# Kernel tuning notes

Hardware: AMD Instinct MI355X
Metric: run time of the kernel (lower is better)

The kernel has to match this reference:

```python
import jax, jax.numpy as jnp
import numpy as np

B, L, ENC, H, E, V, T = 128, 196, 512, 512, 256, 10000, 20


def setup_inputs() -> dict:
    key = jax.random.key(0)
    ks = jax.random.split(key, 24)
    s = 0.02
    n = lambda k, shp: jax.random.normal(k, shp, jnp.float32) * s
    return {
        'img_feat': jax.random.normal(ks[0], (B, L, ENC), jnp.float32),
        'W_h': n(ks[1], (ENC, H)), 'b_h': jnp.zeros((H,), jnp.float32),
        'W_c': n(ks[2], (ENC, H)), 'b_c': jnp.zeros((H,), jnp.float32),
        'W_gate': n(ks[3], (H, ENC)), 'b_gate': jnp.zeros((ENC,), jnp.float32),
        'emb': n(ks[4], (V, E)),
        'W_ae': n(ks[5], (ENC, H)), 'b_ae': jnp.zeros((H,), jnp.float32),
        'W_ad': n(ks[6], (H, H)), 'b_ad': jnp.zeros((H,), jnp.float32),
        'v_att': n(ks[7], (H,)), 'b_v': jnp.zeros((), jnp.float32),
        'W_ih': n(ks[8], (E + ENC, 4 * H)), 'b_ih': jnp.zeros((4 * H,), jnp.float32),
        'W_hh': n(ks[9], (H, 4 * H)), 'b_hh': jnp.zeros((4 * H,), jnp.float32),
        'W_out': n(ks[10], (H, V)), 'b_out': jnp.zeros((V,), jnp.float32),
        'captions': jax.random.randint(ks[11], (B, T), 0, V),
        'max_len': T,
    }


def reference(img_feat, W_h, b_h, W_c, b_c, W_gate, b_gate, emb,
              W_ae, b_ae, W_ad, b_ad, v_att, b_v,
              W_ih, b_ih, W_hh, b_hh, W_out, b_out,
              captions, max_len):
    feat_mean = img_feat.mean(axis=1)                       # [B, ENC]
    h0 = jnp.tanh(feat_mean @ W_h + b_h)                    # [B, H]
    c0 = jnp.tanh(feat_mean @ W_c + b_c)                    # [B, H]
    enc_proj = jnp.einsum('ble,ea->bla', img_feat, W_ae) + b_ae  # [B, L, H]
    emb_seq = emb[captions]                                 # [B, T, E]
    xs = jnp.swapaxes(emb_seq, 0, 1)[:max_len]              # [T, B, E]

    def step(carry, x_t):
        h, c = carry
        # Bahdanau attention
        dec_proj = (h @ W_ad + b_ad)[:, None, :]            # [B, 1, H]
        e = jnp.tanh(enc_proj + dec_proj) @ v_att + b_v     # [B, L]
        alpha = jax.nn.softmax(e, axis=-1)                  # [B, L]
        context = jnp.einsum('bl,ble->be', alpha, img_feat) # [B, ENC]
        gate = jax.nn.sigmoid(h @ W_gate + b_gate)          # [B, ENC]
        x = jnp.concatenate([x_t, context * gate], axis=1)  # [B, E+ENC]
        gates = x @ W_ih + h @ W_hh + (b_ih + b_hh)         # [B, 4H]
        i, f, g, o = jnp.split(gates, 4, axis=1)
        c_new = jax.nn.sigmoid(f) * c + jax.nn.sigmoid(i) * jnp.tanh(g)
        h_new = jax.nn.sigmoid(o) * jnp.tanh(c_new)
        # dropout is identity in eval mode
        out = h_new @ W_out + b_out                         # [B, V]
        return (h_new, c_new), (out, alpha)

    _, (outs, alphas) = jax.lax.scan(step, (h0, c0), xs)
    return jnp.swapaxes(outs, 0, 1), jnp.swapaxes(alphas, 0, 1)
```

## Files before the change

### kernel.cpp

```cpp
#include <hip/hip_runtime.h>
#include <math.h>

typedef unsigned short ushort_t;
typedef __attribute__((ext_vector_type(8))) short bf16x8;
typedef __attribute__((ext_vector_type(4))) short bf16x4;
typedef __attribute__((ext_vector_type(4))) float f32x4;

constexpr int Bb  = 128;
constexpr int Ll  = 196;
constexpr int ENCe= 512;
constexpr int Hh  = 512;
constexpr int Ee  = 256;
constexpr int Vv  = 10000;
constexpr int Tt  = 20;

#define DEV __device__ __forceinline__

DEV float sigm_f(float x) { return 1.f / (1.f + __expf(-x)); }
DEV float tanh_f(float x) {
    x = fminf(fmaxf(x, -15.f), 15.f);
    float e = __expf(2.f * x);
    return (e - 1.f) / (e + 1.f);
}
DEV ushort_t f2bf(float v) {
    unsigned u = __float_as_uint(v);
    return (ushort_t)((u + 0x7FFFu + ((u >> 16) & 1u)) >> 16);
}
DEV float bf2f(ushort_t h) { return __uint_as_float(((unsigned)h) << 16); }

DEV void store_xh(ushort_t* __restrict__ H, ushort_t* __restrict__ L,
                  int b, int k, float v)
{
    size_t idx = (((size_t)(b >> 4) * 40 + (k >> 5)) * 64
                  + ((k >> 3) & 3) * 16 + (b & 15)) * 8 + (k & 7);
    ushort_t hb = f2bf(v);
    H[idx] = hb;
    L[idx] = f2bf(v - bf2f(hb));
}

template<int BN, int TM, int TN, int ACT1, int OUTBF>
__global__ __launch_bounds__(256)
void gemm_k(const float* __restrict__ A, int lda,
            const float* __restrict__ Wk, int ldw,
            const float* __restrict__ bias,
            void* __restrict__ Cv, long long ldc,
            int M, int N, int K)
{
    constexpr int BM = 64, BK = 16;
    constexpr int TX = BN / TN, TY = BM / TM;
    static_assert(TX * TY == 256, "bad tile config");
    __shared__ float As[BK][BM];
    __shared__ float Ws[BK][BN];

    const int tid = threadIdx.x;
    const int tx = tid % TX, ty = tid / TX;
    const int nb = blockIdx.x * BN, mb = blockIdx.y * BM;

    float acc[TM][TN] = {};
    const int am = tid >> 2;
    const int ak = (tid & 3) * 4;
    const int wn = tid % BN;
    const int wk0 = tid / BN;
    constexpr int WKSTEP = 256 / BN;

    for (int k0 = 0; k0 < K; k0 += BK) {
        float4 av = *(const float4*)&A[(size_t)(mb + am) * lda + k0 + ak];
        As[ak + 0][am] = av.x;
        As[ak + 1][am] = av.y;
        As[ak + 2][am] = av.z;
        As[ak + 3][am] = av.w;
        #pragma unroll
        for (int i = 0; i < BK / WKSTEP; ++i) {
            int kw = wk0 + i * WKSTEP;
            Ws[kw][wn] = (nb + wn < N) ? Wk[(size_t)(k0 + kw) * ldw + nb + wn] : 0.f;
        }
        __syncthreads();
        #pragma unroll
        for (int k = 0; k < BK; ++k) {
            float a[TM], w[TN];
            #pragma unroll
            for (int i = 0; i < TM; ++i) a[i] = As[k][ty * TM + i];
            #pragma unroll
            for (int j = 0; j < TN; ++j) w[j] = Ws[k][tx * TN + j];
            #pragma unroll
            for (int i = 0; i < TM; ++i)
                #pragma unroll
                for (int j = 0; j < TN; ++j)
                    acc[i][j] = fmaf(a[i], w[j], acc[i][j]);
        }
        __syncthreads();
    }

    #pragma unroll
    for (int i = 0; i < TM; ++i) {
        int m = mb + ty * TM + i;
        #pragma unroll
        for (int j = 0; j < TN; ++j) {
            int n = nb + tx * TN + j;
            if (n < N) {
                float v = acc[i][j];
                if (bias) v += bias[n];
                if (ACT1 == 1) v = tanh_f(v);
                if (OUTBF) ((ushort_t*)Cv)[(size_t)m * ldc + n] = f2bf(v);
                else       ((float*)Cv)[(size_t)m * ldc + n] = v;
            }
        }
    }
}

template<int MT, int NT, int ACT1, int ACT2, int SPLIT, bool OUTBF, bool PERM,
         bool XSWZ, bool NMINOR, bool W2D>
__global__ __launch_bounds__(256)
void mgemm_pk(const ushort_t* __restrict__ AH, const ushort_t* __restrict__ AL, int aFS,
              const ushort_t* __restrict__ BH, const ushort_t* __restrict__ BL, int bFS,
              const float* __restrict__ bias, const float* __restrict__ bias2, int N1,
              void* __restrict__ Cv, long long ldc, long long ldc2,
              int Nfrags, int Ntot, int nsteps, int bdiv)
{
    int bx, by;
    if (XSWZ) {
        int nwg = gridDim.x, orig = blockIdx.x;
        int xcd = orig & 7, idx = orig >> 3;
        int q = nwg >> 3, r = nwg & 7;
        int lin = (xcd < r ? xcd * (q + 1) : r * (q + 1) + (xcd - r) * q) + idx;
        int l1 = lin / bdiv, l2 = lin - l1 * bdiv;
        bx = NMINOR ? l2 : l1;
        by = NMINOR ? l1 : l2;
    } else { bx = blockIdx.x; by = blockIdx.y; }

    const int wv = threadIdx.x >> 6, lane = threadIdx.x & 63;
    int nf0, mf0;
    if (W2D) {
        nf0 = (bx * 2 + (wv & 1)) * NT;
        mf0 = by * (2 * MT) + (wv >> 1) * MT;
    } else {
        nf0 = (bx * 4 + wv) * NT;
        mf0 = by * MT;
    }
    if (nf0 >= Nfrags) return;
    const int col = lane & 15;
    const int lofs = lane * 8;

    const ushort_t *paH[MT], *paL[MT], *pbH[NT], *pbL[NT];
    #pragma unroll
    for (int mt = 0; mt < MT; ++mt) {
        paH[mt] = AH + (size_t)(mf0 + mt) * aFS + lofs;
        paL[mt] = (SPLIT >= 2) ? (AL + (size_t)(mf0 + mt) * aFS + lofs) : paH[mt];
    }
    #pragma unroll
    for (int ct = 0; ct < NT; ++ct) {
        int nf = nf0 + ct; if (nf > Nfrags - 1) nf = Nfrags - 1;
        pbH[ct] = BH + (size_t)nf * bFS + lofs;
        pbL[ct] = (SPLIT == 3) ? (BL + (size_t)nf * bFS + lofs) : pbH[ct];
    }

    f32x4 acc[MT][NT];
    #pragma unroll
    for (int mt = 0; mt < MT; ++mt)
        #pragma unroll
        for (int ct = 0; ct < NT; ++ct) acc[mt][ct] = (f32x4){0.f, 0.f, 0.f, 0.f};

    auto LOADF = [&](bf16x8 (&A0)[MT], bf16x8 (&A1)[MT],
                     bf16x8 (&B0)[NT], bf16x8 (&B1)[NT], int i) {
        size_t o = (size_t)i * 512;
        #pragma unroll
        for (int mt = 0; mt < MT; ++mt) {
            A0[mt] = *(const bf16x8*)(paH[mt] + o);
            if (SPLIT >= 2) A1[mt] = *(const bf16x8*)(paL[mt] + o);
        }
        #pragma unroll
        for (int ct = 0; ct < NT; ++ct) {
            B0[ct] = *(const bf16x8*)(pbH[ct] + o);
            if (SPLIT == 3) B1[ct] = *(const bf16x8*)(pbL[ct] + o);
        }
    };
    auto COMPF = [&](bf16x8 (&A0)[MT], bf16x8 (&A1)[MT],
                     bf16x8 (&B0)[NT], bf16x8 (&B1)[NT]) {
        #pragma unroll
        for (int mt = 0; mt < MT; ++mt)
            #pragma unroll
            for (int ct = 0; ct < NT; ++ct) {
                acc[mt][ct] = __builtin_amdgcn_mfma_f32_16x16x32_bf16(A0[mt], B0[ct], acc[mt][ct], 0, 0, 0);
                if (SPLIT >= 2)
                    acc[mt][ct] = __builtin_amdgcn_mfma_f32_16x16x32_bf16(A1[mt], B0[ct], acc[mt][ct], 0, 0, 0);
                if (SPLIT == 3)
                    acc[mt][ct] = __builtin_amdgcn_mfma_f32_16x16x32_bf16(A0[mt], B1[ct], acc[mt][ct], 0, 0, 0);
            }
    };

    bf16x8 xa0[MT], xa1[MT], xb0[NT], xb1[NT];
    bf16x8 ya0[MT], ya1[MT], yb0[NT], yb1[NT];
    LOADF(xa0, xa1, xb0, xb1, 0);
    for (int i = 0; i < nsteps; i += 2) {
        LOADF(ya0, ya1, yb0, yb1, i + 1);
        COMPF(xa0, xa1, xb0, xb1);
        if (i + 2 < nsteps) LOADF(xa0, xa1, xb0, xb1, i + 2);
        COMPF(ya0, ya1, yb0, yb1);
    }

    #pragma unroll
    for (int ct = 0; ct < NT; ++ct) {
        const int nc = (nf0 + ct) * 16 + col;
        if (nc >= Ntot) continue;
        const bool ns = ((nf0 + ct) * 16 >= N1);
        float bv = ns ? (bias2 ? bias2[nc - N1] : 0.f) : (bias ? bias[nc] : 0.f);
        const int act = ns ? ACT2 : ACT1;
        #pragma unroll
        for (int mt = 0; mt < MT; ++mt)
            #pragma unroll
            for (int r = 0; r < 4; ++r) {
                int row = (mf0 + mt) * 16 + (lane >> 4) * 4 + r;
                float v = acc[mt][ct][r] + bv;
                if (act == 1)      v = tanh_f(v);
                else if (act == 2) v = sigm_f(v);
                size_t off = PERM ? ((size_t)(row & 127) * ldc + (size_t)(row >> 7) * ldc2 + nc)
                                  : ((size_t)row * ldc + nc);
                if (OUTBF)      ((ushort_t*)Cv)[off] = f2bf(v);
                else if (PERM)  __builtin_nontemporal_store(v, &((float*)Cv)[off]);
                else            ((float*)Cv)[off] = v;
            }
    }
}

template<bool LO>
__global__ __launch_bounds__(256)
void convT_pk(const float* __restrict__ W, int N, int KSr,
              ushort_t* __restrict__ PH, ushort_t* __restrict__ PL,
              int KSfull, int ksOfs, int nfOfs)
{
    int tid = blockIdx.x * 256 + threadIdx.x;
    int lane = tid & 63;
    int rest = tid >> 6;
    int ks = rest % KSr;
    int nf = rest / KSr;
    const float* src = W + (size_t)(ks * 32 + ((lane >> 4) & 3) * 8) * N
                         + nf * 16 + (lane & 15);
    size_t dbase = (((size_t)(nf + nfOfs) * KSfull + ks + ksOfs) * 64 + lane) * 8;
    #pragma unroll
    for (int jj = 0; jj < 8; ++jj) {
        float v = src[(size_t)jj * N];
        ushort_t h = f2bf(v);
        PH[dbase + jj] = h;
        if (LO) PL[dbase + jj] = f2bf(v - bf2f(h));
    }
}

__global__ __launch_bounds__(256)
void convimg_k(const float* __restrict__ img, ushort_t* __restrict__ linH,
               ushort_t* __restrict__ pkH)
{
    int tid = blockIdx.x * 256 + threadIdx.x;
    int lane = tid & 63;
    int rest = tid >> 6;
    int ks = rest & 15, rf = rest >> 4;
    int r = rf * 16 + (lane & 15);
    int k = ks * 32 + ((lane >> 4) & 3) * 8;
    const float* src = img + (size_t)r * 512 + k;
    ushort_t* ld = linH + (size_t)r * 512 + k;
    size_t pidx = (((size_t)rf * 16 + ks) * 64 + lane) * 8;
    #pragma unroll
    for (int jj = 0; jj < 8; ++jj) {
        ushort_t h = f2bf(src[jj]);
        ld[jj] = h;
        pkH[pidx + jj] = h;
    }
}

__global__ void convbf_k(const float* __restrict__ src, ushort_t* __restrict__ dst,
                         long long n)
{
    long long i = (long long)(blockIdx.x * 256 + threadIdx.x) * 4;
    long long stride = (long long)gridDim.x * 1024;
    for (; i + 3 < n; i += stride) {
        float4 v = *(const float4*)&src[i];
        dst[i + 0] = f2bf(v.x); dst[i + 1] = f2bf(v.y);
        dst[i + 2] = f2bf(v.z); dst[i + 3] = f2bf(v.w);
    }
}

__global__ __launch_bounds__(256)
void featmean_k(const float* __restrict__ img, float* __restrict__ fm)
{
    int b = blockIdx.x, tid = threadIdx.x;
    const float* base = img + (size_t)b * Ll * ENCe;
    for (int e = tid; e < ENCe; e += 256) {
        float s = 0.f;
        for (int l = 0; l < Ll; ++l) s += base[l * ENCe + e];
        fm[b * ENCe + e] = s * (1.f / (float)Ll);
    }
}

__global__ void bcomb_k(const float* __restrict__ bih, const float* __restrict__ bhh,
                        float* __restrict__ bc)
{
    int i = blockIdx.x * 256 + threadIdx.x;
    if (i < 4 * Hh) bc[i] = bih[i] + bhh[i];
}

__global__ void hconv_k(const float* __restrict__ h, ushort_t* __restrict__ xhi,
                        ushort_t* __restrict__ xlo)
{
    int i = blockIdx.x * 256 + threadIdx.x;
    if (i >= Bb * Hh) return;
    int b = i / Hh, j = i % Hh;
    store_xh(xhi, xlo, b, 768 + j, h[i]);
}

struct LP {
    const ushort_t *WdgH, *WdgL, *WgH, *WgL;
    const float    *b_ad, *b_gate, *bcomb;
    float          *dgb, *cbuf;
    ushort_t       *xhH, *xhL, *hsH, *hsL;
};

__global__ __launch_bounds__(256)
void ph_dg_k(LP P)
{
    __shared__ f32x4 part[2][64];
    const int beta = blockIdx.x;
    const int tid = threadIdx.x, wv = tid >> 6, lane = tid & 63;
    const int bx = beta >> 3, mf = beta & 7;
    const int nf = bx * 2 + (wv & 1), kh = wv >> 1;
    const int lofs = lane * 8;
    const bool blo = (P.WdgL != nullptr);

    const ushort_t* paH = P.xhH + ((size_t)mf * 40 + 24 + kh * 8) * 512 + lofs;
    const ushort_t* paL = P.xhL + ((size_t)mf * 40 + 24 + kh * 8) * 512 + lofs;
    const ushort_t* pbH = P.WdgH + ((size_t)nf * 16 + kh * 8) * 512 + lofs;
    const ushort_t* pbL = blo ? (P.WdgL + ((size_t)nf * 16 + kh * 8) * 512 + lofs) : pbH;

    f32x4 acc = (f32x4){0.f, 0.f, 0.f, 0.f};
    #pragma unroll
    for (int i = 0; i < 8; ++i) {
        size_t o = (size_t)i * 512;
        bf16x8 A0 = *(const bf16x8*)(paH + o);
        bf16x8 A1 = *(const bf16x8*)(paL + o);
        bf16x8 B0 = *(const bf16x8*)(pbH + o);
        acc = __builtin_amdgcn_mfma_f32_16x16x32_bf16(A0, B0, acc, 0, 0, 0);
        acc = __builtin_amdgcn_mfma_f32_16x16x32_bf16(A1, B0, acc, 0, 0, 0);
        if (blo) {
            bf16x8 B1 = *(const bf16x8*)(pbL + o);
            acc = __builtin_amdgcn_mfma_f32_16x16x32_bf16(A0, B1, acc, 0, 0, 0);
        }
    }

    if (kh == 1) part[wv & 1][lane] = acc;
    __syncthreads();
    if (kh == 0) {
        acc += part[wv & 1][lane];
        int n = nf * 16 + (lane & 15);
        float bv = (n < 512) ? P.b_ad[n] : P.b_gate[n - 512];
        #pragma unroll
        for (int r = 0; r < 4; ++r) {
            int row = mf * 16 + (lane >> 4) * 4 + r;
            float v = acc[r] + bv;
            if (n >= 512) v = sigm_f(v);
            P.dgb[row * 1024 + n] = v;
        }
    }
}

template<bool IMGBF>
__global__ __launch_bounds__(512)
void attn_fused_k(const ushort_t* __restrict__ enc, const float* __restrict__ dgb,
                  const float* __restrict__ v_att,
                  const ushort_t* __restrict__ img_bf, const float* __restrict__ img_f,
                  const float* __restrict__ emb, const int* __restrict__ captions,
                  float* __restrict__ alphas, long long alpha_stride,
                  ushort_t* __restrict__ xhi, ushort_t* __restrict__ xlo, int t)
{
    int b = blockIdx.x, tid = threadIdx.x;
    int wv = tid >> 6, ln = tid & 63;
    __shared__ float es[Ll], red[8];
    __shared__ float ctxp[4][ENCe];

    float dp_r[8], va_r[8];
    {
        const float4* dptr = (const float4*)(dgb + b * 1024 + ln * 8);
        const float4* vptr = (const float4*)(v_att + ln * 8);
        float4 d0 = dptr[0], d1 = dptr[1];
        float4 v0 = vptr[0], v1 = vptr[1];
        dp_r[0] = d0.x; dp_r[1] = d0.y; dp_r[2] = d0.z; dp_r[3] = d0.w;
        dp_r[4] = d1.x; dp_r[5] = d1.y; dp_r[6] = d1.z; dp_r[7] = d1.w;
        va_r[0] = v0.x; va_r[1] = v0.y; va_r[2] = v0.z; va_r[3] = v0.w;
        va_r[4] = v1.x; va_r[5] = v1.y; va_r[6] = v1.z; va_r[7] = v1.w;
    }

    const ushort_t* ep = enc + (size_t)b * Ll * Hh;
    for (int l = wv; l < Ll; l += 8) {
        bf16x8 v8 = *(const bf16x8*)(ep + (size_t)l * Hh + ln * 8);
        float s = 0.f;
        #pragma unroll
        for (int j = 0; j < 8; ++j)
            s += tanh_f(bf2f((ushort_t)v8[j]) + dp_r[j]) * va_r[j];
        #pragma unroll
        for (int o = 32; o; o >>= 1) s += __shfl_xor(s, o);
        if (ln == 0) es[l] = s;
    }
    __syncthreads();

    float v = (tid < Ll) ? es[tid] : -1e30f;
    float m = v;
    #pragma unroll
    for (int o = 32; o; o >>= 1) m = fmaxf(m, __shfl_xor(m, o));
    if (ln == 0) red[wv] = m;
    __syncthreads();
    m = red[0];
    #pragma unroll
    for (int i = 1; i < 8; ++i) m = fmaxf(m, red[i]);
    __syncthreads();
    float p = (tid < Ll) ? __expf(v - m) : 0.f;
    float s = p;
    #pragma unroll
    for (int o = 32; o; o >>= 1) s += __shfl_xor(s, o);
    if (ln == 0) red[wv] = s;
    __syncthreads();
    s = 0.f;
    #pragma unroll
    for (int i = 0; i < 8; ++i) s += red[i];
    float inv = 1.f / s;
    if (tid < Ll) {
        float a = p * inv;
        es[tid] = a;
        alphas[(size_t)b * alpha_stride + tid] = a;
    }
    if (tid < Ee) {
        float xv = emb[(size_t)captions[b * Tt + t] * Ee + tid];
        store_xh(xhi, xlo, b, tid, xv);
    }
    __syncthreads();

    {
        const int g = tid >> 7, tl = tid & 127;
        const int l0 = g * 49;
        float a0 = 0.f, a1 = 0.f, a2 = 0.f, a3 = 0.f;
        if (IMGBF) {
            const ushort_t* ib = img_bf + (size_t)b * Ll * ENCe + tl * 4;
            for (int i = 0; i < 49; ++i) {
                float al = es[l0 + i];
                bf16x4 u = *(const bf16x4*)(ib + (size_t)(l0 + i) * ENCe);
                a0 = fmaf(al, bf2f((ushort_t)u[0]), a0);
                a1 = fmaf(al, bf2f((ushort_t)u[1]), a1);
                a2 = fmaf(al, bf2f((ushort_t)u[2]), a2);
                a3 = fmaf(al, bf2f((ushort_t)u[3]), a3);
            }
        } else {
            const float* ib = img_f + (size_t)b * Ll * ENCe + tl * 4;
            for (int i = 0; i < 49; ++i) {
                float al = es[l0 + i];
                float4 u = *(const float4*)(ib + (size_t)(l0 + i) * ENCe);
                a0 = fmaf(al, u.x, a0);
                a1 = fmaf(al, u.y, a1);
                a2 = fmaf(al, u.z, a2);
                a3 = fmaf(al, u.w, a3);
            }
        }
        f32x4 pv = (f32x4){a0, a1, a2, a3};
        *(f32x4*)&ctxp[g][tl * 4] = pv;
    }
    __syncthreads();

    {
        float cv = ctxp[0][tid] + ctxp[1][tid] + ctxp[2][tid] + ctxp[3][tid];
        float xv = cv * dgb[b * 1024 + 512 + tid];
        store_xh(xhi, xlo, b, 256 + tid, xv);
    }
}

__global__ __launch_bounds__(256)
void ph_gates_k(LP P, int t)
{
    __shared__ f32x4 part[3][4][64];
    const int beta = blockIdx.x;
    const int tid = threadIdx.x, wv = tid >> 6, lane = tid & 63;
    const int jf = beta & 31, mq = beta >> 5;
    const int ks0 = wv * 10, lofs = lane * 8;
    const bool blo = (P.WgL != nullptr);
    constexpr int FS = 40 * 512;

    const ushort_t* paH = P.xhH + ((size_t)mq * 40 + ks0) * 512 + lofs;
    const ushort_t* paL = P.xhL + ((size_t)mq * 40 + ks0) * 512 + lofs;
    const ushort_t *pbH[4], *pbL[4];
    #pragma unroll
    for (int g = 0; g < 4; ++g) {
        size_t off = (size_t)(g * 32 + jf) * FS + (size_t)ks0 * 512 + lofs;
        pbH[g] = P.WgH + off;
        pbL[g] = blo ? (P.WgL + off) : (P.WgH + off);
    }

    f32x4 acc[4];
    #pragma unroll
    for (int g = 0; g < 4; ++g) acc[g] = (f32x4){0.f, 0.f, 0.f, 0.f};

    auto LOADF = [&](bf16x8 (&A)[2], bf16x8 (&B)[4][2], int i) {
        size_t o = (size_t)i * 512;
        A[0] = *(const bf16x8*)(paH + o);
        A[1] = *(const bf16x8*)(paL + o);
        #pragma unroll
        for (int g = 0; g < 4; ++g) {
            B[g][0] = *(const bf16x8*)(pbH[g] + o);
            if (blo) B[g][1] = *(const bf16x8*)(pbL[g] + o);
        }
    };
    auto COMPF = [&](bf16x8 (&A)[2], bf16x8 (&B)[4][2]) {
        #pragma unroll
        for (int g = 0; g < 4; ++g) {
            acc[g] = __builtin_amdgcn_mfma_f32_16x16x32_bf16(A[0], B[g][0], acc[g], 0, 0, 0);
            acc[g] = __builtin_amdgcn_mfma_f32_16x16x32_bf16(A[1], B[g][0], acc[g], 0, 0, 0);
            if (blo)
                acc[g] = __builtin_amdgcn_mfma_f32_16x16x32_bf16(A[0], B[g][1], acc[g], 0, 0, 0);
        }
    };

    bf16x8 xA[2], xB[4][2], yA[2], yB[4][2];
    LOADF(xA, xB, 0);
    for (int i = 0; i < 10; i += 2) {
        LOADF(yA, yB, i + 1);
        COMPF(xA, xB);
        if (i + 2 < 10) LOADF(xA, xB, i + 2);
        COMPF(yA, yB);
    }

    if (wv > 0) {
        #pragma unroll
        for (int g = 0; g < 4; ++g) part[wv - 1][g][lane] = acc[g];
    }
    __syncthreads();
    if (wv == 0) {
        #pragma unroll
        for (int g = 0; g < 4; ++g) {
            acc[g] += part[0][g][lane];
            acc[g] += part[1][g][lane];
            acc[g] += part[2][g][lane];
        }
        const int j = jf * 16 + (lane & 15);
        float bi = P.bcomb[j], bf_ = P.bcomb[512 + j];
        float bg = P.bcomb[1024 + j], bo = P.bcomb[1536 + j];
        #pragma unroll
        for (int r = 0; r < 4; ++r) {
            int b = mq * 16 + (lane >> 4) * 4 + r;
            float ig = sigm_f(acc[0][r] + bi);
            float fg = sigm_f(acc[1][r] + bf_);
            float gg = tanh_f(acc[2][r] + bg);
            float og = sigm_f(acc[3][r] + bo);
            float cn = fg * P.cbuf[b * 512 + j] + ig * gg;
            P.cbuf[b * 512 + j] = cn;
            float hv = og * tanh_f(cn);
            store_xh(P.xhH, P.xhL, b, 768 + j, hv);
            ushort_t hb = f2bf(hv);
            size_t hidx = (((size_t)(t * 8 + (b >> 4)) * 16 + (j >> 5)) * 64
                           + ((j >> 3) & 3) * 16 + (b & 15)) * 8 + (j & 7);
            P.hsH[hidx] = hb;
            P.hsL[hidx] = f2bf(hv - bf2f(hb));
        }
    }
}

extern "C" void kernel_launch(void* const* d_in, const int* in_sizes, int n_in,
                              void* d_out, int out_size, void* d_ws, size_t ws_size,
                              hipStream_t stream)
{
    const float* img    = (const float*)d_in[0];
    const float* W_h    = (const float*)d_in[1];
    const float* b_h    = (const float*)d_in[2];
    const float* W_c    = (const float*)d_in[3];
    const float* b_c    = (const float*)d_in[4];
    const float* W_gate = (const float*)d_in[5];
    const float* b_gate = (const float*)d_in[6];
    const float* emb    = (const float*)d_in[7];
    const float* W_ae   = (const float*)d_in[8];
    const float* b_ae   = (const float*)d_in[9];
    const float* W_ad   = (const float*)d_in[10];
    const float* b_ad   = (const float*)d_in[11];
    const float* v_att  = (const float*)d_in[12];
    const float* W_ih   = (const float*)d_in[14];
    const float* b_ih   = (const float*)d_in[15];
    const float* W_hh   = (const float*)d_in[16];
    const float* b_hh   = (const float*)d_in[17];
    const float* W_out  = (const float*)d_in[18];
    const float* b_out  = (const float*)d_in[19];
    const int* captions = (const int*)d_in[20];

    float* out    = (float*)d_out;
    float* alphas = out + (size_t)Bb * Tt * Vv;

    char* p = (char*)d_ws;
    auto alloc = [&](size_t bytes) -> char* {
        char* r = p; p += (bytes + 255) & ~(size_t)255; return r;
    };
    const size_t szEnc   = (size_t)Bb * Ll * Hh * 2;
    const size_t szWout  = (size_t)625 * 16 * 512 * 2;
    const size_t szWg    = (size_t)128 * 40 * 512 * 2;
    const size_t szWdg   = (size_t)64 * 16 * 512 * 2;
    const size_t szWae   = (size_t)32 * 16 * 512 * 2;
    const size_t szXh    = (size_t)8 * 40 * 512 * 2;
    const size_t szHseq  = (size_t)160 * 16 * 512 * 2;
    const size_t szImg   = (size_t)Bb * Ll * ENCe * 2;

    ushort_t* enc_hi  = (ushort_t*)alloc(szEnc);
    ushort_t* WoutPkH = (ushort_t*)alloc(szWout);
    ushort_t* WgPkH   = (ushort_t*)alloc(szWg);
    ushort_t* WdgPkH  = (ushort_t*)alloc(szWdg);
    ushort_t* WaePkH  = (ushort_t*)alloc(szWae);
    ushort_t* xhPkH   = (ushort_t*)alloc(szXh);
    ushort_t* xhPkL   = (ushort_t*)alloc(szXh);
    ushort_t* hseqPkH = (ushort_t*)alloc(szHseq);
    ushort_t* hseqPkL = (ushort_t*)alloc(szHseq);
    float*    cbuf    = (float*)alloc((size_t)Bb * Hh * 4);
    float*    dgb     = (float*)alloc((size_t)Bb * 1024 * 4);
    float*    S       = (float*)alloc((size_t)Bb * 1024 * 4);
    float*    bcomb   = (float*)alloc(4 * Hh * 4);

    auto tryAlloc = [&](size_t bytes) -> char* {
        size_t used = (size_t)(p - (char*)d_ws);
        size_t rounded = (bytes + 255) & ~(size_t)255;
        if (used + rounded > ws_size) return nullptr;
        return alloc(bytes);
    };
    ushort_t* WoutPkL = (ushort_t*)tryAlloc(szWout);
    ushort_t* WgPkL   = (ushort_t*)tryAlloc(szWg);
    ushort_t* WdgPkL  = (ushort_t*)tryAlloc(szWdg);
    ushort_t* imgLin  = (ushort_t*)tryAlloc(szImg);
    ushort_t* imgPk   = (ushort_t*)tryAlloc(szImg);

    float* fm  = S;
    float* h0b = S + Bb * ENCe;

    dim3 blk(256);
    const int NOSPLIT = 0x40000000;
    const int aFSh    = 16 * 512;

    if (WoutPkL) convT_pk<true ><<<2500, blk, 0, stream>>>(W_out, Vv, 16, WoutPkH, WoutPkL, 16, 0, 0);
    else         convT_pk<false><<<2500, blk, 0, stream>>>(W_out, Vv, 16, WoutPkH, nullptr, 16, 0, 0);
    if (WgPkL) {
        convT_pk<true ><<<768, blk, 0, stream>>>(W_ih, 2048, 24, WgPkH, WgPkL, 40, 0, 0);
        convT_pk<true ><<<512, blk, 0, stream>>>(W_hh, 2048, 16, WgPkH, WgPkL, 40, 24, 0);
    } else {
        convT_pk<false><<<768, blk, 0, stream>>>(W_ih, 2048, 24, WgPkH, nullptr, 40, 0, 0);
        convT_pk<false><<<512, blk, 0, stream>>>(W_hh, 2048, 16, WgPkH, nullptr, 40, 24, 0);
    }
    if (WdgPkL) {
        convT_pk<true ><<<128, blk, 0, stream>>>(W_ad,   Hh, 16, WdgPkH, WdgPkL, 16, 0, 0);
        convT_pk<true ><<<128, blk, 0, stream>>>(W_gate, Hh, 16, WdgPkH, WdgPkL, 16, 0, 32);
    } else {
        convT_pk<false><<<128, blk, 0, stream>>>(W_ad,   Hh, 16, WdgPkH, nullptr, 16, 0, 0);
        convT_pk<false><<<128, blk, 0, stream>>>(W_gate, Hh, 16, WdgPkH, nullptr, 16, 0, 32);
    }
    convT_pk<false><<<128, blk, 0, stream>>>(W_ae, Hh, 16, WaePkH, nullptr, 16, 0, 0);

    bcomb_k<<<(4 * Hh + 255) / 256, blk, 0, stream>>>(b_ih, b_hh, bcomb);
    featmean_k<<<Bb, blk, 0, stream>>>(img, fm);

    gemm_k<32, 2, 4, 1, 0><<<dim3(Hh / 32, Bb / 64), blk, 0, stream>>>(
        fm, ENCe, W_h, Hh, b_h, h0b, Hh, Bb, Hh, ENCe);
    gemm_k<32, 2, 4, 1, 0><<<dim3(Hh / 32, Bb / 64), blk, 0, stream>>>(
        fm, ENCe, W_c, Hh, b_c, cbuf, Hh, Bb, Hh, ENCe);
    hconv_k<<<(Bb * Hh + 255) / 256, blk, 0, stream>>>(h0b, xhPkH, xhPkL);

    if (imgPk && imgLin) {
        convimg_k<<<6272, blk, 0, stream>>>(img, imgLin, imgPk);
        mgemm_pk<4, 4, 0, 0, 1, true, false, true, true, true><<<dim3(784), blk, 0, stream>>>(
            imgPk, nullptr, aFSh, WaePkH, nullptr, aFSh, b_ae, nullptr, NOSPLIT,
            enc_hi, Hh, 0, 32, Hh, 16, 4);
    } else {
        if (imgLin) convbf_k<<<2048, blk, 0, stream>>>(img, imgLin, (long long)Bb * Ll * ENCe);
        gemm_k<64, 4, 4, 0, 1><<<dim3(Hh / 64, (Bb * Ll) / 64), blk, 0, stream>>>(
            img, ENCe, W_ae, Hh, b_ae, enc_hi, Hh, Bb * Ll, Hh, ENCe);
    }

    LP P;
    P.WdgH = WdgPkH; P.WdgL = WdgPkL; P.WgH = WgPkH; P.WgL = WgPkL;
    P.b_ad = b_ad; P.b_gate = b_gate; P.bcomb = bcomb;
    P.dgb = dgb; P.cbuf = cbuf;
    P.xhH = xhPkH; P.xhL = xhPkL; P.hsH = hseqPkH; P.hsL = hseqPkL;

    for (int t = 0; t < Tt; ++t) {
        ph_dg_k<<<256, blk, 0, stream>>>(P);
        if (imgLin)
            attn_fused_k<true ><<<Bb, dim3(512), 0, stream>>>(
                enc_hi, dgb, v_att, imgLin, nullptr, emb, captions,
                alphas + (size_t)t * Ll, (long long)Tt * Ll, xhPkH, xhPkL, t);
        else
            attn_fused_k<false><<<Bb, dim3(512), 0, stream>>>(
                enc_hi, dgb, v_att, nullptr, img, emb, captions,
                alphas + (size_t)t * Ll, (long long)Tt * Ll, xhPkH, xhPkL, t);
        ph_gates_k<<<256, blk, 0, stream>>>(P, t);
    }

    if (WoutPkL)
        mgemm_pk<4, 4, 0, 0, 3, false, true, true, false, true><<<dim3(79 * 20), blk, 0, stream>>>(
            hseqPkH, hseqPkL, aFSh, WoutPkH, WoutPkL, aFSh,
            b_out, nullptr, NOSPLIT, out, (long long)Tt * Vv, (long long)Vv,
            625, Vv, 16, 20);
    else
        mgemm_pk<4, 4, 0, 0, 2, false, true, true, false, true><<<dim3(79 * 20), blk, 0, stream>>>(
            hseqPkH, hseqPkL, aFSh, WoutPkH, nullptr, aFSh,
            b_out, nullptr, NOSPLIT, out, (long long)Tt * Vv, (long long)Vv,
            625, Vv, 16, 20);
}
```

Measured before the change: 1.107 ms.

## Drop bf16 low-part weight splits and fuse small prologue kernels

```diff
diff --git a/kernel.cpp b/kernel.cpp
--- a/kernel.cpp
+++ b/kernel.cpp
@@ -104,6 +104,69 @@
                 if (OUTBF) ((ushort_t*)Cv)[(size_t)m * ldc + n] = f2bf(v);
                 else       ((float*)Cv)[(size_t)m * ldc + n] = v;
             }
+        }
+    }
+}
+
+__global__ __launch_bounds__(256)
+void gemmxh_k(const float* __restrict__ A, int lda,
+              const float* __restrict__ Wk, int ldw,
+              const float* __restrict__ bias,
+              ushort_t* __restrict__ xhH, ushort_t* __restrict__ xhL,
+              int N, int K)
+{
+    constexpr int BM = 64, BK = 16, BN = 32, TM = 2, TN = 4;
+    constexpr int TX = BN / TN;
+    __shared__ float As[BK][BM];
+    __shared__ float Ws[BK][BN];
+
+    const int tid = threadIdx.x;
+    const int tx = tid % TX, ty = tid / TX;
+    const int nb = blockIdx.x * BN, mb = blockIdx.y * BM;
+
+    float acc[TM][TN] = {};
+    const int am = tid >> 2;
+    const int ak = (tid & 3) * 4;
+    const int wn = tid % BN;
+    const int wk0 = tid / BN;
+    constexpr int WKSTEP = 256 / BN;
+
+    for (int k0 = 0; k0 < K; k0 += BK) {
+        float4 av = *(const float4*)&A[(size_t)(mb + am) * lda + k0 + ak];
+        As[ak + 0][am] = av.x;
+        As[ak + 1][am] = av.y;
+        As[ak + 2][am] = av.z;
+        As[ak + 3][am] = av.w;
+        #pragma unroll
+        for (int i = 0; i < BK / WKSTEP; ++i) {
+            int kw = wk0 + i * WKSTEP;
+            Ws[kw][wn] = Wk[(size_t)(k0 + kw) * ldw + nb + wn];
+        }
+        __syncthreads();
+        #pragma unroll
+        for (int k = 0; k < BK; ++k) {
+            float a[TM], w[TN];
+            #pragma unroll
+            for (int i = 0; i < TM; ++i) a[i] = As[k][ty * TM + i];
+            #pragma unroll
+            for (int j = 0; j < TN; ++j) w[j] = Ws[k][tx * TN + j];
+            #pragma unroll
+            for (int i = 0; i < TM; ++i)
+                #pragma unroll
+                for (int j = 0; j < TN; ++j)
+                    acc[i][j] = fmaf(a[i], w[j], acc[i][j]);
+        }
+        __syncthreads();
+    }
+
+    #pragma unroll
+    for (int i = 0; i < TM; ++i) {
+        int m = mb + ty * TM + i;
+        #pragma unroll
+        for (int j = 0; j < TN; ++j) {
+            int n = nb + tx * TN + j;
+            float v = tanh_f(acc[i][j] + bias[n]);
+            store_xh(xhH, xhL, m, 768 + n, v);
         }
     }
 }
@@ -279,9 +342,15 @@
 }
 
 __global__ __launch_bounds__(256)
-void featmean_k(const float* __restrict__ img, float* __restrict__ fm)
+void featmean_k(const float* __restrict__ img, float* __restrict__ fm,
+                const float* __restrict__ bih, const float* __restrict__ bhh,
+                float* __restrict__ bc)
 {
     int b = blockIdx.x, tid = threadIdx.x;
+    if (b < 8) {
+        int i = b * 256 + tid;
+        bc[i] = bih[i] + bhh[i];
+    }
     const float* base = img + (size_t)b * Ll * ENCe;
     for (int e = tid; e < ENCe; e += 256) {
         float s = 0.f;
@@ -290,24 +359,8 @@
     }
 }
 
-__global__ void bcomb_k(const float* __restrict__ bih, const float* __restrict__ bhh,
-                        float* __restrict__ bc)
-{
-    int i = blockIdx.x * 256 + threadIdx.x;
-    if (i < 4 * Hh) bc[i] = bih[i] + bhh[i];
-}
-
-__global__ void hconv_k(const float* __restrict__ h, ushort_t* __restrict__ xhi,
-                        ushort_t* __restrict__ xlo)
-{
-    int i = blockIdx.x * 256 + threadIdx.x;
-    if (i >= Bb * Hh) return;
-    int b = i / Hh, j = i % Hh;
-    store_xh(xhi, xlo, b, 768 + j, h[i]);
-}
-
 struct LP {
-    const ushort_t *WdgH, *WdgL, *WgH, *WgL;
+    const ushort_t *WdgH, *WgH;
     const float    *b_ad, *b_gate, *bcomb;
     float          *dgb, *cbuf;
     ushort_t       *xhH, *xhL, *hsH, *hsL;
@@ -322,12 +375,10 @@
     const int bx = beta >> 3, mf = beta & 7;
     const int nf = bx * 2 + (wv & 1), kh = wv >> 1;
     const int lofs = lane * 8;
-    const bool blo = (P.WdgL != nullptr);
 
     const ushort_t* paH = P.xhH + ((size_t)mf * 40 + 24 + kh * 8) * 512 + lofs;
     const ushort_t* paL = P.xhL + ((size_t)mf * 40 + 24 + kh * 8) * 512 + lofs;
     const ushort_t* pbH = P.WdgH + ((size_t)nf * 16 + kh * 8) * 512 + lofs;
-    const ushort_t* pbL = blo ? (P.WdgL + ((size_t)nf * 16 + kh * 8) * 512 + lofs) : pbH;
 
     f32x4 acc = (f32x4){0.f, 0.f, 0.f, 0.f};
     #pragma unroll
@@ -338,10 +389,6 @@
         bf16x8 B0 = *(const bf16x8*)(pbH + o);
         acc = __builtin_amdgcn_mfma_f32_16x16x32_bf16(A0, B0, acc, 0, 0, 0);
         acc = __builtin_amdgcn_mfma_f32_16x16x32_bf16(A1, B0, acc, 0, 0, 0);
-        if (blo) {
-            bf16x8 B1 = *(const bf16x8*)(pbL + o);
-            acc = __builtin_amdgcn_mfma_f32_16x16x32_bf16(A0, B1, acc, 0, 0, 0);
-        }
     }
 
     if (kh == 1) part[wv & 1][lane] = acc;
@@ -470,49 +517,40 @@
 __global__ __launch_bounds__(256)
 void ph_gates_k(LP P, int t)
 {
-    __shared__ f32x4 part[3][4][64];
+    __shared__ f32x4 part[4][4][64];
     const int beta = blockIdx.x;
     const int tid = threadIdx.x, wv = tid >> 6, lane = tid & 63;
     const int jf = beta & 31, mq = beta >> 5;
     const int ks0 = wv * 10, lofs = lane * 8;
-    const bool blo = (P.WgL != nullptr);
     constexpr int FS = 40 * 512;
 
     const ushort_t* paH = P.xhH + ((size_t)mq * 40 + ks0) * 512 + lofs;
     const ushort_t* paL = P.xhL + ((size_t)mq * 40 + ks0) * 512 + lofs;
-    const ushort_t *pbH[4], *pbL[4];
-    #pragma unroll
-    for (int g = 0; g < 4; ++g) {
-        size_t off = (size_t)(g * 32 + jf) * FS + (size_t)ks0 * 512 + lofs;
-        pbH[g] = P.WgH + off;
-        pbL[g] = blo ? (P.WgL + off) : (P.WgH + off);
-    }
+    const ushort_t *pbH[4];
+    #pragma unroll
+    for (int g = 0; g < 4; ++g)
+        pbH[g] = P.WgH + (size_t)(g * 32 + jf) * FS + (size_t)ks0 * 512 + lofs;
 
     f32x4 acc[4];
     #pragma unroll
     for (int g = 0; g < 4; ++g) acc[g] = (f32x4){0.f, 0.f, 0.f, 0.f};
 
-    auto LOADF = [&](bf16x8 (&A)[2], bf16x8 (&B)[4][2], int i) {
+    auto LOADF = [&](bf16x8 (&A)[2], bf16x8 (&B)[4], int i) {
         size_t o = (size_t)i * 512;
         A[0] = *(const bf16x8*)(paH + o);
         A[1] = *(const bf16x8*)(paL + o);
         #pragma unroll
+        for (int g = 0; g < 4; ++g) B[g] = *(const bf16x8*)(pbH[g] + o);
+    };
+    auto COMPF = [&](bf16x8 (&A)[2], bf16x8 (&B)[4]) {
+        #pragma unroll
         for (int g = 0; g < 4; ++g) {
-            B[g][0] = *(const bf16x8*)(pbH[g] + o);
-            if (blo) B[g][1] = *(const bf16x8*)(pbL[g] + o);
+            acc[g] = __builtin_amdgcn_mfma_f32_16x16x32_bf16(A[0], B[g], acc[g], 0, 0, 0);
+            acc[g] = __builtin_amdgcn_mfma_f32_16x16x32_bf16(A[1], B[g], acc[g], 0, 0, 0);
         }
     };
-    auto COMPF = [&](bf16x8 (&A)[2], bf16x8 (&B)[4][2]) {
-        #pragma unroll
-        for (int g = 0; g < 4; ++g) {
-            acc[g] = __builtin_amdgcn_mfma_f32_16x16x32_bf16(A[0], B[g][0], acc[g], 0, 0, 0);
-            acc[g] = __builtin_amdgcn_mfma_f32_16x16x32_bf16(A[1], B[g][0], acc[g], 0, 0, 0);
-            if (blo)
-                acc[g] = __builtin_amdgcn_mfma_f32_16x16x32_bf16(A[0], B[g][1], acc[g], 0, 0, 0);
-        }
-    };
-
-    bf16x8 xA[2], xB[4][2], yA[2], yB[4][2];
+
+    bf16x8 xA[2], xB[4], yA[2], yB[4];
     LOADF(xA, xB, 0);
     for (int i = 0; i < 10; i += 2) {
         LOADF(yA, yB, i + 1);
@@ -521,39 +559,33 @@
         COMPF(yA, yB);
     }
 
-    if (wv > 0) {
-        #pragma unroll
-        for (int g = 0; g < 4; ++g) part[wv - 1][g][lane] = acc[g];
-    }
+    #pragma unroll
+    for (int g = 0; g < 4; ++g) part[wv][g][lane] = acc[g];
     __syncthreads();
-    if (wv == 0) {
-        #pragma unroll
-        for (int g = 0; g < 4; ++g) {
-            acc[g] += part[0][g][lane];
-            acc[g] += part[1][g][lane];
-            acc[g] += part[2][g][lane];
-        }
-        const int j = jf * 16 + (lane & 15);
-        float bi = P.bcomb[j], bf_ = P.bcomb[512 + j];
-        float bg = P.bcomb[1024 + j], bo = P.bcomb[1536 + j];
-        #pragma unroll
-        for (int r = 0; r < 4; ++r) {
-            int b = mq * 16 + (lane >> 4) * 4 + r;
-            float ig = sigm_f(acc[0][r] + bi);
-            float fg = sigm_f(acc[1][r] + bf_);
-            float gg = tanh_f(acc[2][r] + bg);
-            float og = sigm_f(acc[3][r] + bo);
-            float cn = fg * P.cbuf[b * 512 + j] + ig * gg;
-            P.cbuf[b * 512 + j] = cn;
-            float hv = og * tanh_f(cn);
-            store_xh(P.xhH, P.xhL, b, 768 + j, hv);
-            ushort_t hb = f2bf(hv);
-            size_t hidx = (((size_t)(t * 8 + (b >> 4)) * 16 + (j >> 5)) * 64
-                           + ((j >> 3) & 3) * 16 + (b & 15)) * 8 + (j & 7);
-            P.hsH[hidx] = hb;
-            P.hsL[hidx] = f2bf(hv - bf2f(hb));
-        }
-    }
+
+    const int jl = tid & 15, bl = tid >> 4;
+    const int lane2 = (bl >> 2) * 16 + jl, r2 = bl & 3;
+    float g4[4];
+    #pragma unroll
+    for (int g = 0; g < 4; ++g)
+        g4[g] = part[0][g][lane2][r2] + part[1][g][lane2][r2]
+              + part[2][g][lane2][r2] + part[3][g][lane2][r2];
+
+    const int j = jf * 16 + jl;
+    const int b = mq * 16 + bl;
+    float ig = sigm_f(g4[0] + P.bcomb[j]);
+    float fg = sigm_f(g4[1] + P.bcomb[512 + j]);
+    float gg = tanh_f(g4[2] + P.bcomb[1024 + j]);
+    float og = sigm_f(g4[3] + P.bcomb[1536 + j]);
+    float cn = fg * P.cbuf[b * 512 + j] + ig * gg;
+    P.cbuf[b * 512 + j] = cn;
+    float hv = og * tanh_f(cn);
+    store_xh(P.xhH, P.xhL, b, 768 + j, hv);
+    ushort_t hb = f2bf(hv);
+    size_t hidx = (((size_t)(t * 8 + (b >> 4)) * 16 + (j >> 5)) * 64
+                   + ((j >> 3) & 3) * 16 + (b & 15)) * 8 + (j & 7);
+    P.hsH[hidx] = hb;
+    P.hsL[hidx] = f2bf(hv - bf2f(hb));
 }
 
 extern "C" void kernel_launch(void* const* d_in, const int* in_sizes, int n_in,
@@ -608,7 +640,7 @@
     ushort_t* hseqPkL = (ushort_t*)alloc(szHseq);
     float*    cbuf    = (float*)alloc((size_t)Bb * Hh * 4);
     float*    dgb     = (float*)alloc((size_t)Bb * 1024 * 4);
-    float*    S       = (float*)alloc((size_t)Bb * 1024 * 4);
+    float*    fm      = (float*)alloc((size_t)Bb * ENCe * 4);
     float*    bcomb   = (float*)alloc(4 * Hh * 4);
 
     auto tryAlloc = [&](size_t bytes) -> char* {
@@ -617,45 +649,25 @@
         if (used + rounded > ws_size) return nullptr;
         return alloc(bytes);
     };
-    ushort_t* WoutPkL = (ushort_t*)tryAlloc(szWout);
-    ushort_t* WgPkL   = (ushort_t*)tryAlloc(szWg);
-    ushort_t* WdgPkL  = (ushort_t*)tryAlloc(szWdg);
-    ushort_t* imgLin  = (ushort_t*)tryAlloc(szImg);
-    ushort_t* imgPk   = (ushort_t*)tryAlloc(szImg);
-
-    float* fm  = S;
-    float* h0b = S + Bb * ENCe;
+    ushort_t* imgLin = (ushort_t*)tryAlloc(szImg);
+    ushort_t* imgPk  = (ushort_t*)tryAlloc(szImg);
 
     dim3 blk(256);
     const int NOSPLIT = 0x40000000;
     const int aFSh    = 16 * 512;
 
-    if (WoutPkL) convT_pk<true ><<<2500, blk, 0, stream>>>(W_out, Vv, 16, WoutPkH, WoutPkL, 16, 0, 0);
-    else         convT_pk<false><<<2500, blk, 0, stream>>>(W_out, Vv, 16, WoutPkH, nullptr, 16, 0, 0);
-    if (WgPkL) {
-        convT_pk<true ><<<768, blk, 0, stream>>>(W_ih, 2048, 24, WgPkH, WgPkL, 40, 0, 0);
-        convT_pk<true ><<<512, blk, 0, stream>>>(W_hh, 2048, 16, WgPkH, WgPkL, 40, 24, 0);
-    } else {
-        convT_pk<false><<<768, blk, 0, stream>>>(W_ih, 2048, 24, WgPkH, nullptr, 40, 0, 0);
-        convT_pk<false><<<512, blk, 0, stream>>>(W_hh, 2048, 16, WgPkH, nullptr, 40, 24, 0);
-    }
-    if (WdgPkL) {
-        convT_pk<true ><<<128, blk, 0, stream>>>(W_ad,   Hh, 16, WdgPkH, WdgPkL, 16, 0, 0);
-        convT_pk<true ><<<128, blk, 0, stream>>>(W_gate, Hh, 16, WdgPkH, WdgPkL, 16, 0, 32);
-    } else {
-        convT_pk<false><<<128, blk, 0, stream>>>(W_ad,   Hh, 16, WdgPkH, nullptr, 16, 0, 0);
-        convT_pk<false><<<128, blk, 0, stream>>>(W_gate, Hh, 16, WdgPkH, nullptr, 16, 0, 32);
-    }
+    convT_pk<false><<<2500, blk, 0, stream>>>(W_out, Vv, 16, WoutPkH, nullptr, 16, 0, 0);
+    convT_pk<false><<<768, blk, 0, stream>>>(W_ih, 2048, 24, WgPkH, nullptr, 40, 0, 0);
+    convT_pk<false><<<512, blk, 0, stream>>>(W_hh, 2048, 16, WgPkH, nullptr, 40, 24, 0);
+    convT_pk<false><<<128, blk, 0, stream>>>(W_ad,   Hh, 16, WdgPkH, nullptr, 16, 0, 0);
+    convT_pk<false><<<128, blk, 0, stream>>>(W_gate, Hh, 16, WdgPkH, nullptr, 16, 0, 32);
     convT_pk<false><<<128, blk, 0, stream>>>(W_ae, Hh, 16, WaePkH, nullptr, 16, 0, 0);
 
-    bcomb_k<<<(4 * Hh + 255) / 256, blk, 0, stream>>>(b_ih, b_hh, bcomb);
-    featmean_k<<<Bb, blk, 0, stream>>>(img, fm);
-
-    gemm_k<32, 2, 4, 1, 0><<<dim3(Hh / 32, Bb / 64), blk, 0, stream>>>(
-        fm, ENCe, W_h, Hh, b_h, h0b, Hh, Bb, Hh, ENCe);
-    gemm_k<32, 2, 4, 1, 0><<<dim3(Hh / 32, Bb / 64), blk, 0, stream>>>(
+    featmean_k<<<Bb, blk, 0, stream>>>(img, fm, b_ih, b_hh, bcomb);
+
+    gemmxh_k<<<dim3(16, 2), blk, 0, stream>>>(fm, ENCe, W_h, Hh, b_h, xhPkH, xhPkL, Hh, ENCe);
+    gemm_k<32, 2, 4, 1, 0><<<dim3(16, 2), blk, 0, stream>>>(
         fm, ENCe, W_c, Hh, b_c, cbuf, Hh, Bb, Hh, ENCe);
-    hconv_k<<<(Bb * Hh + 255) / 256, blk, 0, stream>>>(h0b, xhPkH, xhPkL);
 
     if (imgPk && imgLin) {
         convimg_k<<<6272, blk, 0, stream>>>(img, imgLin, imgPk);
@@ -669,7 +681,7 @@
     }
 
     LP P;
-    P.WdgH = WdgPkH; P.WdgL = WdgPkL; P.WgH = WgPkH; P.WgL = WgPkL;
+    P.WdgH = WdgPkH; P.WgH = WgPkH;
     P.b_ad = b_ad; P.b_gate = b_gate; P.bcomb = bcomb;
     P.dgb = dgb; P.cbuf = cbuf;
     P.xhH = xhPkH; P.xhL = xhPkL; P.hsH = hseqPkH; P.hsL = hseqPkL;
@@ -687,14 +699,8 @@
         ph_gates_k<<<256, blk, 0, stream>>>(P, t);
     }
 
-    if (WoutPkL)
-        mgemm_pk<4, 4, 0, 0, 3, false, true, true, false, true><<<dim3(79 * 20), blk, 0, stream>>>(
-            hseqPkH, hseqPkL, aFSh, WoutPkH, WoutPkL, aFSh,
-            b_out, nullptr, NOSPLIT, out, (long long)Tt * Vv, (long long)Vv,
-            625, Vv, 16, 20);
-    else
-        mgemm_pk<4, 4, 0, 0, 2, false, true, true, false, true><<<dim3(79 * 20), blk, 0, stream>>>(
-            hseqPkH, hseqPkL, aFSh, WoutPkH, nullptr, aFSh,
-            b_out, nullptr, NOSPLIT, out, (long long)Tt * Vv, (long long)Vv,
-            625, Vv, 16, 20);
-}
+    mgemm_pk<4, 4, 0, 0, 2, false, true, true, false, true><<<dim3(79 * 20), blk, 0, stream>>>(
+        hseqPkH, hseqPkL, aFSh, WoutPkH, nullptr, aFSh,
+        b_out, nullptr, NOSPLIT, out, (long long)Tt * Vv, (long long)Vv,
+        625, Vv, 16, 20);
+}
```

New measurement: 992.4 us. -10.4%, faster.
